# Performance work log

Hardware: AMD Instinct MI355X
Metric: run time of the kernel (lower is better)

The kernel has to match this reference:

```python
import jax, jax.numpy as jnp
import numpy as np

TAU = 0.1          # temperature from init_kwargs
EPS = 1e-8         # torch.nn.CosineSimilarity default eps


def setup_inputs() -> dict:
    key = jax.random.key(0)
    k1, k2, k3 = jax.random.split(key, 3)
    B, D = 2048, 128
    return {
        "z_i": jax.random.normal(k1, (B, D), dtype=jnp.float32),
        "z_j": jax.random.normal(k2, (B, D), dtype=jnp.float32),
        "y": jax.random.randint(k3, (B,), 0, 10, dtype=jnp.int64),
    }


def reference(z_i, z_j, y):
    # p: (2N, D)
    p = jnp.concatenate([z_i, z_j], axis=0)
    n2 = p.shape[0]
    # Cosine similarity via norms + single GEMM (same math as pairwise
    # CosineSimilarity: dot / max(||a||*||b||, eps)), then temperature scale.
    norms = jnp.linalg.norm(p, axis=1)                      # (2N,)
    sim = (p @ p.T) / jnp.maximum(norms[:, None] * norms[None, :], EPS) / TAU

    # Positive mask: same label, diagonal removed.
    y2 = jnp.concatenate([y, y], axis=0)                    # (2N,)
    off_diag = 1.0 - jnp.eye(n2, dtype=sim.dtype)           # logit mask
    mask = (y2[:, None] == y2[None, :]).astype(sim.dtype) * off_diag

    # Masked log-softmax over each row (self excluded from denominator).
    exp_logits = jnp.exp(sim) * off_diag
    log_prob = sim - jnp.log(exp_logits.sum(axis=1, keepdims=True))

    mean_log_prob_pos = (mask * log_prob).sum(axis=1) / mask.sum(axis=1)
    return -mean_log_prob_pos.mean()
```

## Files before the change

kernel.cpp:

```cpp
#include <hip/hip_runtime.h>

#define N2 4096
#define D 128
#define TAU_INV 10.0f
#define E2SCALE 14.4269504088896340736f
#define BM 256
#define BN 256
#define NT (BN / 32)
#define GEMM_BLOCKS ((N2 / BM) * (N2 / BN))
#define NCLS 10
#define CGRP 16
#define CROWS (N2 / CGRP)
#define CB (NCLS * CGRP)

typedef __attribute__((ext_vector_type(8))) short bf16x8;
typedef __attribute__((ext_vector_type(16))) float floatx16;

__device__ __forceinline__ short f2bf(float f) {
    unsigned u = __float_as_uint(f);
    u = (u + 0x7fff + ((u >> 16) & 1)) >> 16;
    return (short)u;
}
__device__ __forceinline__ float bf2f(short s) {
    return __uint_as_float(((unsigned)(unsigned short)s) << 16);
}

__global__ __launch_bounds__(64) void prep_kernel(const float* __restrict__ zi,
                                                  const float* __restrict__ zj,
                                                  short* __restrict__ qb,
                                                  short* __restrict__ qb2,
                                                  float* __restrict__ se_g,
                                                  float* __restrict__ S) {
    int row = blockIdx.x;
    int lane = threadIdx.x;
    const float* src = (row < 2048) ? (zi + row * D) : (zj + (row - 2048) * D);
    float2 v = ((const float2*)src)[lane];
    float ss = v.x * v.x + v.y * v.y;
    #pragma unroll
    for (int m = 1; m < 64; m <<= 1) ss += __shfl_xor(ss, m);
    float inv = 1.0f / sqrtf(ss);
    short2 o;
    o.x = f2bf(v.x * inv);
    o.y = f2bf(v.y * inv);
    ((short2*)(qb + row * D))[lane] = o;
    int addr2 = (row >> 5) * 4096 + (lane >> 2) * 256 + (row & 31) * 8 + 2 * (lane & 3);
    *(short2*)(qb2 + addr2) = o;
    if (lane == 0) se_g[row] = 0.f;
    if (row == 0)
        for (int k = lane; k < NCLS * D + 2 * NCLS; k += 64) S[k] = 0.f;
}

__global__ __launch_bounds__(512) void main_kernel(const short* __restrict__ qb,
                                                   const short* __restrict__ qb2,
                                                   const long long* __restrict__ y,
                                                   float* __restrict__ se_g,
                                                   float* __restrict__ S) {
    int tid = threadIdx.x;
    int wave = tid >> 6;
    int lane = tid & 63;

    if (blockIdx.x >= GEMM_BLOCKS) {
        __shared__ float shS[512];
        __shared__ float shT[8];
        __shared__ float shC[4];
        int cb = blockIdx.x - GEMM_BLOCKS;
        int c  = cb / CGRP;
        int g  = cb % CGRP;
        int d  = tid & 127;
        int rg = tid >> 7;
        int r0 = g * CROWS + rg * (CROWS / 4);

        float sS = 0.f, sT = 0.f, cnt = 0.f;
        #pragma unroll 4
        for (int i = 0; i < CROWS / 4; ++i) {
            int r = r0 + i;
            bool m = ((int)y[r & 2047] == c);
            float q = bf2f(qb[r * D + d]);
            sS += m ? q : 0.f;
            sT += m ? q * q : 0.f;
            cnt += m ? 1.f : 0.f;
        }

        shS[tid] = sS;
        #pragma unroll
        for (int m = 1; m < 64; m <<= 1) sT += __shfl_xor(sT, m);
        if (lane == 0) shT[wave] = sT;
        if (d == 0) shC[rg] = cnt;
        __syncthreads();
        if (tid < 128)
            atomicAdd(&S[c * D + tid],
                      shS[tid] + shS[tid + 128] + shS[tid + 256] + shS[tid + 384]);
        if (tid == 0) {
            float t8 = 0.f;
            #pragma unroll
            for (int w = 0; w < 8; ++w) t8 += shT[w];
            atomicAdd(&S[NCLS * D + c], t8);
            atomicAdd(&S[NCLS * D + NCLS + c], shC[0] + shC[1] + shC[2] + shC[3]);
        }
        return;
    }

    __shared__ short ldsB[BN * D];
    int gb = blockIdx.x;
    int col  = lane & 31;
    int half = lane >> 5;
    int it = gb >> 4;
    int js = gb & 15;
    int rbase = it * BM + wave * 32;
    int jbase = js * BN;

    {
        const bf16x8* src = (const bf16x8*)(qb2 + js * (BN * D));
        bf16x8* dst = (bf16x8*)ldsB;
        #pragma unroll
        for (int i = 0; i < 8; ++i) dst[tid + 512 * i] = src[tid + 512 * i];
    }

    const short* ap = qb2 + ((rbase >> 5) * 4096) + lane * 8;
    bf16x8 af[8];
    #pragma unroll
    for (int k = 0; k < 8; ++k) af[k] = *(const bf16x8*)(ap + k * 512);

    float se[16];
    #pragma unroll
    for (int r = 0; r < 16; ++r) se[r] = 0.f;

    __syncthreads();

    const bf16x8* lb = (const bf16x8*)ldsB;
    #pragma unroll
    for (int t = 0; t < NT; ++t) {
        int j0 = jbase + t * 32;

        floatx16 acc;
        #pragma unroll
        for (int r = 0; r < 16; ++r) acc[r] = 0.f;
        #pragma unroll
        for (int k = 0; k < 8; ++k)
            acc = __builtin_amdgcn_mfma_f32_32x32x16_bf16(
                af[k], lb[t * 512 + k * 64 + lane], acc, 0, 0, 0);

        if (j0 == rbase) {
            int jcol = j0 + col;
            #pragma unroll
            for (int r = 0; r < 16; ++r) {
                int rowr = rbase + (r & 3) + 8 * (r >> 2) + 4 * half;
                float e = __builtin_amdgcn_exp2f(acc[r] * E2SCALE);
                se[r] += (rowr == jcol) ? 0.f : e;
            }
        } else {
            #pragma unroll
            for (int r = 0; r < 16; ++r)
                se[r] += __builtin_amdgcn_exp2f(acc[r] * E2SCALE);
        }
    }

    #pragma unroll
    for (int r = 0; r < 16; ++r) {
        float a = se[r];
        #pragma unroll
        for (int m = 1; m < 32; m <<= 1) a += __shfl_xor(a, m);
        if (col == 0) {
            int rowr = rbase + (r & 3) + 8 * (r >> 2) + 4 * half;
            atomicAdd(&se_g[rowr], a);
        }
    }
}

__global__ __launch_bounds__(256) void finish_kernel(const float* __restrict__ se_g,
                                                     const float* __restrict__ S,
                                                     float* __restrict__ out) {
    int tid = threadIdx.x;
    int wave = tid >> 6;
    int lane = tid & 63;

    float P = 0.f;
    for (int c = wave; c < NCLS; c += 4) {
        float2 sv = ((const float2*)(S + c * D))[lane];
        float s2 = sv.x * sv.x + sv.y * sv.y;
        #pragma unroll
        for (int m = 1; m < 64; m <<= 1) s2 += __shfl_xor(s2, m);
        float n = S[NCLS * D + NCLS + c];
        P += (n >= 2.0f) ? (s2 - S[NCLS * D + c]) * TAU_INV / (n - 1.0f) : 0.f;
    }

    float L = 0.f;
    for (int i = tid; i < N2; i += 256) L += __logf(se_g[i]);
    #pragma unroll
    for (int m = 1; m < 64; m <<= 1) L += __shfl_xor(L, m);

    __shared__ float red[8];
    if (lane == 0) { red[wave] = L; red[4 + wave] = P; }
    __syncthreads();
    if (tid == 0) {
        float Ls = red[0] + red[1] + red[2] + red[3];
        float Ps = red[4] + red[5] + red[6] + red[7];
        out[0] = (Ls - Ps) * (1.0f / (float)N2);
    }
}

extern "C" void kernel_launch(void* const* d_in, const int* in_sizes, int n_in,
                              void* d_out, int out_size, void* d_ws, size_t ws_size,
                              hipStream_t stream) {
    const float*     zi = (const float*)d_in[0];
    const float*     zj = (const float*)d_in[1];
    const long long* y  = (const long long*)d_in[2];
    float* out = (float*)d_out;

    char* ws = (char*)d_ws;
    short* qb   = (short*)ws;
    short* qb2  = qb + N2 * D;
    float* se_g = (float*)(ws + 2 * N2 * D * sizeof(short));
    float* S    = se_g + N2;

    prep_kernel<<<N2, 64, 0, stream>>>(zi, zj, qb, qb2, se_g, S);
    main_kernel<<<GEMM_BLOCKS + CB, 512, 0, stream>>>(qb, qb2, y, se_g, S);
    finish_kernel<<<1, 256, 0, stream>>>(se_g, S, out);
}
```

Before: 88.26 us.

## Fuse normalization into GEMM blocks and replace atomics with partial buffers

Removes the separate prep kernel. Each GEMM block now loads the fp32 rows itself, normalizes them, converts them to bf16 into LDS and registers, and the class-sum blocks normalize their own rows. Atomic accumulation into se_g and S is replaced by per-block partial outputs that the finish kernel sums, so no zero-initialization or atomics are needed. The cost is redundant normalization work: each row is normalized 16 times across blocks and fp32 global reads double. In exchange, one launch and the qb/qb2 intermediate round trip go away.

Result: no change. 89.82 us (+1.8%).

```diff
diff --git a/kernel.cpp b/kernel.cpp
--- a/kernel.cpp
+++ b/kernel.cpp
@@ -7,11 +7,13 @@
 #define BM 256
 #define BN 256
 #define NT (BN / 32)
-#define GEMM_BLOCKS ((N2 / BM) * (N2 / BN))
+#define NIT (N2 / BM)
+#define GEMM_BLOCKS (NIT * NIT)
 #define NCLS 10
 #define CGRP 16
 #define CROWS (N2 / CGRP)
 #define CB (NCLS * CGRP)
+#define PCW 130
 
 typedef __attribute__((ext_vector_type(8))) short bf16x8;
 typedef __attribute__((ext_vector_type(16))) float floatx16;
@@ -25,101 +27,126 @@
     return __uint_as_float(((unsigned)(unsigned short)s) << 16);
 }
 
-__global__ __launch_bounds__(64) void prep_kernel(const float* __restrict__ zi,
-                                                  const float* __restrict__ zj,
-                                                  short* __restrict__ qb,
-                                                  short* __restrict__ qb2,
-                                                  float* __restrict__ se_g,
-                                                  float* __restrict__ S) {
-    int row = blockIdx.x;
-    int lane = threadIdx.x;
-    const float* src = (row < 2048) ? (zi + row * D) : (zj + (row - 2048) * D);
-    float2 v = ((const float2*)src)[lane];
-    float ss = v.x * v.x + v.y * v.y;
-    #pragma unroll
-    for (int m = 1; m < 64; m <<= 1) ss += __shfl_xor(ss, m);
-    float inv = 1.0f / sqrtf(ss);
-    short2 o;
-    o.x = f2bf(v.x * inv);
-    o.y = f2bf(v.y * inv);
-    ((short2*)(qb + row * D))[lane] = o;
-    int addr2 = (row >> 5) * 4096 + (lane >> 2) * 256 + (row & 31) * 8 + 2 * (lane & 3);
-    *(short2*)(qb2 + addr2) = o;
-    if (lane == 0) se_g[row] = 0.f;
-    if (row == 0)
-        for (int k = lane; k < NCLS * D + 2 * NCLS; k += 64) S[k] = 0.f;
-}
-
-__global__ __launch_bounds__(512) void main_kernel(const short* __restrict__ qb,
-                                                   const short* __restrict__ qb2,
+__global__ __launch_bounds__(512) void main_kernel(const float* __restrict__ zi,
+                                                   const float* __restrict__ zj,
                                                    const long long* __restrict__ y,
-                                                   float* __restrict__ se_g,
-                                                   float* __restrict__ S) {
+                                                   float* __restrict__ pse,
+                                                   float* __restrict__ pcls) {
+    __shared__ short ldsB[BN * D];
     int tid = threadIdx.x;
     int wave = tid >> 6;
     int lane = tid & 63;
 
     if (blockIdx.x >= GEMM_BLOCKS) {
-        __shared__ float shS[512];
-        __shared__ float shT[8];
-        __shared__ float shC[4];
+        float* shf = (float*)ldsB;
         int cb = blockIdx.x - GEMM_BLOCKS;
         int c  = cb / CGRP;
         int g  = cb % CGRP;
-        int d  = tid & 127;
-        int rg = tid >> 7;
-        int r0 = g * CROWS + rg * (CROWS / 4);
-
-        float sS = 0.f, sT = 0.f, cnt = 0.f;
-        #pragma unroll 4
-        for (int i = 0; i < CROWS / 4; ++i) {
-            int r = r0 + i;
+
+        float sSx = 0.f, sSy = 0.f, sT = 0.f, cnt = 0.f;
+        for (int i = 0; i < CROWS / 8; ++i) {
+            int r = g * CROWS + wave * (CROWS / 8) + i;
+            const float* src = (r < 2048) ? (zi + r * D) : (zj + (r - 2048) * D);
+            float2 v = ((const float2*)src)[lane];
+            float ss = v.x * v.x + v.y * v.y;
+            #pragma unroll
+            for (int m = 1; m < 64; m <<= 1) ss += __shfl_xor(ss, m);
+            float inv = 1.0f / sqrtf(ss);
+            float qx = bf2f(f2bf(v.x * inv));
+            float qy = bf2f(f2bf(v.y * inv));
             bool m = ((int)y[r & 2047] == c);
-            float q = bf2f(qb[r * D + d]);
-            sS += m ? q : 0.f;
-            sT += m ? q * q : 0.f;
+            sSx += m ? qx : 0.f;
+            sSy += m ? qy : 0.f;
+            sT  += m ? (qx * qx + qy * qy) : 0.f;
             cnt += m ? 1.f : 0.f;
         }
-
-        shS[tid] = sS;
+        shf[wave * D + 2 * lane]     = sSx;
+        shf[wave * D + 2 * lane + 1] = sSy;
         #pragma unroll
         for (int m = 1; m < 64; m <<= 1) sT += __shfl_xor(sT, m);
-        if (lane == 0) shT[wave] = sT;
-        if (d == 0) shC[rg] = cnt;
+        if (lane == 0) { shf[1024 + wave] = sT; shf[1032 + wave] = cnt; }
         __syncthreads();
-        if (tid < 128)
-            atomicAdd(&S[c * D + tid],
-                      shS[tid] + shS[tid + 128] + shS[tid + 256] + shS[tid + 384]);
-        if (tid == 0) {
-            float t8 = 0.f;
-            #pragma unroll
-            for (int w = 0; w < 8; ++w) t8 += shT[w];
-            atomicAdd(&S[NCLS * D + c], t8);
-            atomicAdd(&S[NCLS * D + NCLS + c], shC[0] + shC[1] + shC[2] + shC[3]);
+        if (tid < D) {
+            float s = 0.f;
+            #pragma unroll
+            for (int w = 0; w < 8; ++w) s += shf[w * D + tid];
+            pcls[cb * PCW + tid] = s;
+        } else if (tid == D) {
+            float s = 0.f;
+            #pragma unroll
+            for (int w = 0; w < 8; ++w) s += shf[1024 + w];
+            pcls[cb * PCW + 128] = s;
+        } else if (tid == D + 1) {
+            float s = 0.f;
+            #pragma unroll
+            for (int w = 0; w < 8; ++w) s += shf[1032 + w];
+            pcls[cb * PCW + 129] = s;
         }
         return;
     }
 
-    __shared__ short ldsB[BN * D];
     int gb = blockIdx.x;
     int col  = lane & 31;
     int half = lane >> 5;
     int it = gb >> 4;
     int js = gb & 15;
     int rbase = it * BM + wave * 32;
-    int jbase = js * BN;
-
+
+    #pragma unroll
+    for (int pass = 0; pass < 2; ++pass) {
+        int rl = pass * 128 + (tid >> 2);
+        int q  = tid & 3;
+        int gr = js * BN + rl;
+        const float* srcb = (gr < 2048) ? (zi + gr * D) : (zj + (gr - 2048) * D);
+        float4 b0[8];
+        float part = 0.f;
+        #pragma unroll
+        for (int j = 0; j < 8; ++j) {
+            float4 u = *(const float4*)(srcb + q * 32 + j * 4);
+            part += u.x * u.x + u.y * u.y + u.z * u.z + u.w * u.w;
+            b0[j] = u;
+        }
+        part += __shfl_xor(part, 1);
+        part += __shfl_xor(part, 2);
+        float invb = 1.0f / sqrtf(part);
+        #pragma unroll
+        for (int jj = 0; jj < 4; ++jj) {
+            float4 u = b0[2 * jj], v = b0[2 * jj + 1];
+            bf16x8 t;
+            t[0] = f2bf(u.x * invb); t[1] = f2bf(u.y * invb);
+            t[2] = f2bf(u.z * invb); t[3] = f2bf(u.w * invb);
+            t[4] = f2bf(v.x * invb); t[5] = f2bf(v.y * invb);
+            t[6] = f2bf(v.z * invb); t[7] = f2bf(v.w * invb);
+            *(bf16x8*)&ldsB[(rl >> 5) * 4096 + (q * 4 + jj) * 256 + (rl & 31) * 8] = t;
+        }
+    }
+
+    bf16x8 af[8];
     {
-        const bf16x8* src = (const bf16x8*)(qb2 + js * (BN * D));
-        bf16x8* dst = (bf16x8*)ldsB;
-        #pragma unroll
-        for (int i = 0; i < 8; ++i) dst[tid + 512 * i] = src[tid + 512 * i];
-    }
-
-    const short* ap = qb2 + ((rbase >> 5) * 4096) + lane * 8;
-    bf16x8 af[8];
-    #pragma unroll
-    for (int k = 0; k < 8; ++k) af[k] = *(const bf16x8*)(ap + k * 512);
+        int grow = rbase + col;
+        const float* srca = (grow < 2048) ? (zi + grow * D) : (zj + (grow - 2048) * D);
+        float4 a0[8], a1[8];
+        float ssq = 0.f;
+        #pragma unroll
+        for (int k = 0; k < 8; ++k) {
+            float4 u = *(const float4*)(srca + k * 16 + half * 8);
+            float4 v = *(const float4*)(srca + k * 16 + half * 8 + 4);
+            ssq += u.x * u.x + u.y * u.y + u.z * u.z + u.w * u.w
+                 + v.x * v.x + v.y * v.y + v.z * v.z + v.w * v.w;
+            a0[k] = u; a1[k] = v;
+        }
+        ssq += __shfl_xor(ssq, 32);
+        float inv = 1.0f / sqrtf(ssq);
+        #pragma unroll
+        for (int k = 0; k < 8; ++k) {
+            bf16x8 t;
+            t[0] = f2bf(a0[k].x * inv); t[1] = f2bf(a0[k].y * inv);
+            t[2] = f2bf(a0[k].z * inv); t[3] = f2bf(a0[k].w * inv);
+            t[4] = f2bf(a1[k].x * inv); t[5] = f2bf(a1[k].y * inv);
+            t[6] = f2bf(a1[k].z * inv); t[7] = f2bf(a1[k].w * inv);
+            af[k] = t;
+        }
+    }
 
     float se[16];
     #pragma unroll
@@ -130,7 +157,7 @@
     const bf16x8* lb = (const bf16x8*)ldsB;
     #pragma unroll
     for (int t = 0; t < NT; ++t) {
-        int j0 = jbase + t * 32;
+        int j0 = js * BN + t * 32;
 
         floatx16 acc;
         #pragma unroll
@@ -162,39 +189,52 @@
         for (int m = 1; m < 32; m <<= 1) a += __shfl_xor(a, m);
         if (col == 0) {
             int rowr = rbase + (r & 3) + 8 * (r >> 2) + 4 * half;
-            atomicAdd(&se_g[rowr], a);
-        }
-    }
-}
-
-__global__ __launch_bounds__(256) void finish_kernel(const float* __restrict__ se_g,
-                                                     const float* __restrict__ S,
+            pse[rowr * NIT + js] = a;
+        }
+    }
+}
+
+__global__ __launch_bounds__(512) void finish_kernel(const float* __restrict__ pse,
+                                                     const float* __restrict__ pcls,
                                                      float* __restrict__ out) {
+    __shared__ float red[16];
     int tid = threadIdx.x;
     int wave = tid >> 6;
     int lane = tid & 63;
 
+    float L = 0.f;
+    for (int r = tid; r < N2; r += 512) {
+        float s = 0.f;
+        #pragma unroll
+        for (int js = 0; js < NIT; ++js) s += pse[r * NIT + js];
+        L += __logf(s);
+    }
+    #pragma unroll
+    for (int m = 1; m < 64; m <<= 1) L += __shfl_xor(L, m);
+
     float P = 0.f;
-    for (int c = wave; c < NCLS; c += 4) {
-        float2 sv = ((const float2*)(S + c * D))[lane];
-        float s2 = sv.x * sv.x + sv.y * sv.y;
+    for (int c = wave; c < NCLS; c += 8) {
+        float Sx = 0.f, Sy = 0.f, T = 0.f, n = 0.f;
+        #pragma unroll
+        for (int g = 0; g < CGRP; ++g) {
+            const float* p = pcls + (c * CGRP + g) * PCW;
+            Sx += p[2 * lane];
+            Sy += p[2 * lane + 1];
+            T  += p[128];
+            n  += p[129];
+        }
+        float s2 = Sx * Sx + Sy * Sy;
         #pragma unroll
         for (int m = 1; m < 64; m <<= 1) s2 += __shfl_xor(s2, m);
-        float n = S[NCLS * D + NCLS + c];
-        P += (n >= 2.0f) ? (s2 - S[NCLS * D + c]) * TAU_INV / (n - 1.0f) : 0.f;
-    }
-
-    float L = 0.f;
-    for (int i = tid; i < N2; i += 256) L += __logf(se_g[i]);
-    #pragma unroll
-    for (int m = 1; m < 64; m <<= 1) L += __shfl_xor(L, m);
-
-    __shared__ float red[8];
-    if (lane == 0) { red[wave] = L; red[4 + wave] = P; }
+        P += (n >= 2.0f) ? (s2 - T) * TAU_INV / (n - 1.0f) : 0.f;
+    }
+
+    if (lane == 0) { red[wave] = L; red[8 + wave] = P; }
     __syncthreads();
     if (tid == 0) {
-        float Ls = red[0] + red[1] + red[2] + red[3];
-        float Ps = red[4] + red[5] + red[6] + red[7];
+        float Ls = 0.f, Ps = 0.f;
+        #pragma unroll
+        for (int w = 0; w < 8; ++w) { Ls += red[w]; Ps += red[8 + w]; }
         out[0] = (Ls - Ps) * (1.0f / (float)N2);
     }
 }
@@ -208,12 +248,9 @@
     float* out = (float*)d_out;
 
     char* ws = (char*)d_ws;
-    short* qb   = (short*)ws;
-    short* qb2  = qb + N2 * D;
-    float* se_g = (float*)(ws + 2 * N2 * D * sizeof(short));
-    float* S    = se_g + N2;
-
-    prep_kernel<<<N2, 64, 0, stream>>>(zi, zj, qb, qb2, se_g, S);
-    main_kernel<<<GEMM_BLOCKS + CB, 512, 0, stream>>>(qb, qb2, y, se_g, S);
-    finish_kernel<<<1, 256, 0, stream>>>(se_g, S, out);
-}
+    float* pse  = (float*)ws;
+    float* pcls = pse + N2 * NIT;
+
+    main_kernel<<<GEMM_BLOCKS + CB, 512, 0, stream>>>(zi, zj, y, pse, pcls);
+    finish_kernel<<<1, 512, 0, stream>>>(pse, pcls, out);
+}
```

## Exploit symmetry of similarity matrix to compute only upper-triangular tiles

Applied to the files above, without the earlier changes.

Since sim is symmetric, only the upper-triangular block tiles are launched (136 instead of 256 GEMM blocks). Off-diagonal tiles also produce column sums of exp, accumulated in shared memory via LDS atomics, which supply the transposed tile's row sums. Per-tile partial row sums go into a (row, tile) buffer instead of global atomics, and the finish kernel sums and logs them. This roughly halves MFMA and exp work at the cost of extra shuffles, LDS atomics and a serial block-index decode.

Result: faster. 83.69 us (median of 2 runs) (-5.2%).

```diff
diff --git a/kernel.cpp b/kernel.cpp
--- a/kernel.cpp
+++ b/kernel.cpp
@@ -7,7 +7,8 @@
 #define BM 256
 #define BN 256
 #define NT (BN / 32)
-#define GEMM_BLOCKS ((N2 / BM) * (N2 / BN))
+#define NIT (N2 / BM)
+#define GEMM_BLOCKS (NIT * (NIT + 1) / 2)
 #define NCLS 10
 #define CGRP 16
 #define CROWS (N2 / CGRP)
@@ -29,7 +30,6 @@
                                                   const float* __restrict__ zj,
                                                   short* __restrict__ qb,
                                                   short* __restrict__ qb2,
-                                                  float* __restrict__ se_g,
                                                   float* __restrict__ S) {
     int row = blockIdx.x;
     int lane = threadIdx.x;
@@ -45,7 +45,6 @@
     ((short2*)(qb + row * D))[lane] = o;
     int addr2 = (row >> 5) * 4096 + (lane >> 2) * 256 + (row & 31) * 8 + 2 * (lane & 3);
     *(short2*)(qb2 + addr2) = o;
-    if (lane == 0) se_g[row] = 0.f;
     if (row == 0)
         for (int k = lane; k < NCLS * D + 2 * NCLS; k += 64) S[k] = 0.f;
 }
@@ -53,7 +52,7 @@
 __global__ __launch_bounds__(512) void main_kernel(const short* __restrict__ qb,
                                                    const short* __restrict__ qb2,
                                                    const long long* __restrict__ y,
-                                                   float* __restrict__ se_g,
+                                                   float* __restrict__ pse,
                                                    float* __restrict__ S) {
     int tid = threadIdx.x;
     int wave = tid >> 6;
@@ -101,13 +100,14 @@
     }
 
     __shared__ short ldsB[BN * D];
-    int gb = blockIdx.x;
+    __shared__ float colsum[BN];
+    int b = blockIdx.x, it = 0;
+    while (b >= NIT - it) { b -= NIT - it; ++it; }
+    int js = it + b;
     int col  = lane & 31;
     int half = lane >> 5;
-    int it = gb >> 4;
-    int js = gb & 15;
     int rbase = it * BM + wave * 32;
-    int jbase = js * BN;
+    bool offdiag = (it != js);
 
     {
         const bf16x8* src = (const bf16x8*)(qb2 + js * (BN * D));
@@ -115,6 +115,7 @@
         #pragma unroll
         for (int i = 0; i < 8; ++i) dst[tid + 512 * i] = src[tid + 512 * i];
     }
+    if (tid < BN) colsum[tid] = 0.f;
 
     const short* ap = qb2 + ((rbase >> 5) * 4096) + lane * 8;
     bf16x8 af[8];
@@ -130,7 +131,7 @@
     const bf16x8* lb = (const bf16x8*)ldsB;
     #pragma unroll
     for (int t = 0; t < NT; ++t) {
-        int j0 = jbase + t * 32;
+        int j0 = js * BN + t * 32;
 
         floatx16 acc;
         #pragma unroll
@@ -149,9 +150,17 @@
                 se[r] += (rowr == jcol) ? 0.f : e;
             }
         } else {
+            float cs = 0.f;
             #pragma unroll
-            for (int r = 0; r < 16; ++r)
-                se[r] += __builtin_amdgcn_exp2f(acc[r] * E2SCALE);
+            for (int r = 0; r < 16; ++r) {
+                float e = __builtin_amdgcn_exp2f(acc[r] * E2SCALE);
+                se[r] += e;
+                cs += e;
+            }
+            if (offdiag) {
+                cs += __shfl_xor(cs, 32);
+                if (half == 0) atomicAdd(&colsum[t * 32 + col], cs);
+            }
         }
     }
 
@@ -162,20 +171,37 @@
         for (int m = 1; m < 32; m <<= 1) a += __shfl_xor(a, m);
         if (col == 0) {
             int rowr = rbase + (r & 3) + 8 * (r >> 2) + 4 * half;
-            atomicAdd(&se_g[rowr], a);
-        }
-    }
-}
-
-__global__ __launch_bounds__(256) void finish_kernel(const float* __restrict__ se_g,
+            pse[rowr * NIT + js] = a;
+        }
+    }
+
+    if (offdiag) {
+        __syncthreads();
+        if (tid < BN)
+            pse[(js * BN + tid) * NIT + it] = colsum[tid];
+    }
+}
+
+__global__ __launch_bounds__(512) void finish_kernel(const float* __restrict__ pse,
                                                      const float* __restrict__ S,
                                                      float* __restrict__ out) {
+    __shared__ float red[16];
     int tid = threadIdx.x;
     int wave = tid >> 6;
     int lane = tid & 63;
 
+    float L = 0.f;
+    for (int r = tid; r < N2; r += 512) {
+        float s = 0.f;
+        #pragma unroll
+        for (int k = 0; k < NIT; ++k) s += pse[r * NIT + k];
+        L += __logf(s);
+    }
+    #pragma unroll
+    for (int m = 1; m < 64; m <<= 1) L += __shfl_xor(L, m);
+
     float P = 0.f;
-    for (int c = wave; c < NCLS; c += 4) {
+    for (int c = wave; c < NCLS; c += 8) {
         float2 sv = ((const float2*)(S + c * D))[lane];
         float s2 = sv.x * sv.x + sv.y * sv.y;
         #pragma unroll
@@ -184,17 +210,12 @@
         P += (n >= 2.0f) ? (s2 - S[NCLS * D + c]) * TAU_INV / (n - 1.0f) : 0.f;
     }
 
-    float L = 0.f;
-    for (int i = tid; i < N2; i += 256) L += __logf(se_g[i]);
-    #pragma unroll
-    for (int m = 1; m < 64; m <<= 1) L += __shfl_xor(L, m);
-
-    __shared__ float red[8];
-    if (lane == 0) { red[wave] = L; red[4 + wave] = P; }
+    if (lane == 0) { red[wave] = L; red[8 + wave] = P; }
     __syncthreads();
     if (tid == 0) {
-        float Ls = red[0] + red[1] + red[2] + red[3];
-        float Ps = red[4] + red[5] + red[6] + red[7];
+        float Ls = 0.f, Ps = 0.f;
+        #pragma unroll
+        for (int w = 0; w < 8; ++w) { Ls += red[w]; Ps += red[8 + w]; }
         out[0] = (Ls - Ps) * (1.0f / (float)N2);
     }
 }
@@ -210,10 +231,10 @@
     char* ws = (char*)d_ws;
     short* qb   = (short*)ws;
     short* qb2  = qb + N2 * D;
-    float* se_g = (float*)(ws + 2 * N2 * D * sizeof(short));
-    float* S    = se_g + N2;
-
-    prep_kernel<<<N2, 64, 0, stream>>>(zi, zj, qb, qb2, se_g, S);
-    main_kernel<<<GEMM_BLOCKS + CB, 512, 0, stream>>>(qb, qb2, y, se_g, S);
-    finish_kernel<<<1, 256, 0, stream>>>(se_g, S, out);
-}
+    float* pse  = (float*)(ws + 2 * N2 * D * sizeof(short));
+    float* S    = pse + N2 * NIT;
+
+    prep_kernel<<<N2, 64, 0, stream>>>(zi, zj, qb, qb2, S);
+    main_kernel<<<GEMM_BLOCKS + CB, 512, 0, stream>>>(qb, qb2, y, pse, S);
+    finish_kernel<<<1, 512, 0, stream>>>(pse, S, out);
+}
```
